# Performance work log

Measured on AMD Instinct MI355X. Metric: run time of the kernel, lower is better.

The kernel has to match this reference:

```python
import jax, jax.numpy as jnp
import numpy as np

D_K = 64

def setup_inputs() -> dict:
    key = jax.random.key(0)
    k1, k2, k3, k4 = jax.random.split(key, 4)
    hidden_states = jax.random.normal(k1, (2, 16, 128, 16, 16), dtype=jnp.float32)
    # nn.Linear(hidden, d, bias=False); stored as [in, out] for x @ W
    w_q = jax.random.normal(k2, (128, 64), dtype=jnp.float32) * 0.05
    w_k = jax.random.normal(k3, (128, 64), dtype=jnp.float32) * 0.05
    w_v = jax.random.normal(k4, (128, 64), dtype=jnp.float32) * 0.05
    return {"hidden_states": hidden_states, "w_q": w_q, "w_k": w_k, "w_v": w_v}

def reference(hidden_states, w_q, w_k, w_v):
    # (B, T, C, H, W) -> (B, T, H, W, C) -> (N, C)
    x = jnp.transpose(hidden_states, (0, 1, 3, 4, 2))
    x = x.reshape(-1, x.shape[-1])                      # [N, C], N = B*T*H*W
    q = x @ w_q                                          # [N, d_k]
    k = x @ w_k                                          # [N, d_k]
    v = x @ w_v                                          # [N, d_v]
    scores = (q @ k.T) / jnp.sqrt(jnp.asarray(D_K, x.dtype))  # [N, N]
    attn = jax.nn.softmax(scores, axis=1)                # softmax over dim=1
    out = attn @ v                                       # [N, d_v]
    return out
```

## Files before the change

kernel.cpp:

```cpp
#include <hip/hip_runtime.h>
#include <hip/hip_bf16.h>

typedef float f32x4 __attribute__((ext_vector_type(4)));
typedef short bf16x8 __attribute__((ext_vector_type(8)));

#define MFMA32 __builtin_amdgcn_mfma_f32_16x16x32_bf16

__device__ __forceinline__ unsigned short f2bf(float f) {
  union { float f; unsigned u; } v; v.f = f;
  unsigned u = v.u;
  u += 0x7FFFu + ((u >> 16) & 1u);
  return (unsigned short)(u >> 16);
}

__device__ __forceinline__ bf16x8 pack8_bf16(float a, float b, float c, float d,
                                             float e, float f, float g, float h) {
  union { bf16x8 v; __hip_bfloat162 p[4]; } u;
  u.p[0] = __float22bfloat162_rn(make_float2(a, b));
  u.p[1] = __float22bfloat162_rn(make_float2(c, d));
  u.p[2] = __float22bfloat162_rn(make_float2(e, f));
  u.p[3] = __float22bfloat162_rn(make_float2(g, h));
  return u.v;
}

__device__ __forceinline__ void stage16(const unsigned short* gbase,
                                        unsigned short* lbase, int lane) {
#if __has_builtin(__builtin_amdgcn_global_load_lds)
  __builtin_amdgcn_global_load_lds(
      (const __attribute__((address_space(1))) void*)(gbase + lane * 8),
      (__attribute__((address_space(3))) void*)lbase, 16, 0, 0);
#else
  *(bf16x8*)(lbase + lane * 8) = *(const bf16x8*)(gbase + lane * 8);
#endif
}

__global__ __launch_bounds__(256) void qkv_kernel(
    const float* __restrict__ hs,
    const float* __restrict__ wq, const float* __restrict__ wk,
    const float* __restrict__ wv,
    unsigned short* __restrict__ qb, unsigned short* __restrict__ kpack,
    unsigned short* __restrict__ vpack)
{
  __shared__ __align__(16) float Wl[128 * 64];
  __shared__ float xs[32 * 129];
  const int t = threadIdx.x;
  const int mat = blockIdx.y;
  const float* __restrict__ W = (mat == 0) ? wq : (mat == 1) ? wk : wv;
  #pragma unroll
  for (int i = 0; i < 8; ++i) {
    *(f32x4*)(Wl + i * 1024 + t * 4) = *(const f32x4*)(W + i * 1024 + t * 4);
  }
  const int n0 = blockIdx.x * 32;
  const int bt = n0 >> 8;
  const int sp0 = n0 & 255;
  {
    const float* __restrict__ src = hs + (size_t)bt * 32768 + sp0;
    const int s = t & 31, cb = t >> 5;
    #pragma unroll
    for (int i = 0; i < 16; ++i) {
      const int c = i * 8 + cb;
      xs[s * 129 + c] = src[c * 256 + s];
    }
  }
  __syncthreads();
  const int s = t & 31, g = t >> 5;
  float acc[8];
  #pragma unroll
  for (int j = 0; j < 8; ++j) acc[j] = 0.f;
  #pragma unroll 4
  for (int c = 0; c < 128; ++c) {
    const float xv = xs[s * 129 + c];
    const f32x4 w0 = *(const f32x4*)(Wl + c * 64 + g * 8);
    const f32x4 w1 = *(const f32x4*)(Wl + c * 64 + g * 8 + 4);
    acc[0] += xv * w0[0]; acc[1] += xv * w0[1];
    acc[2] += xv * w0[2]; acc[3] += xv * w0[3];
    acc[4] += xv * w1[0]; acc[5] += xv * w1[1];
    acc[6] += xv * w1[2]; acc[7] += xv * w1[3];
  }
  const int n = n0 + s;
  const float SCALE = 1.4426950408889634f / 8.0f;
  if (mat == 0) {
    #pragma unroll
    for (int j = 0; j < 8; ++j) qb[n * 64 + g * 8 + j] = f2bf(acc[j] * SCALE);
  } else if (mat == 1) {
    const int kvb32 = n >> 5, kvl = n & 31;
    const int ti = (kvl >> 2) & 1;
    const int lowk = ((kvl >> 3) << 2) | (kvl & 3);
    const int h = g >> 2, quadk = g & 3;
    unsigned short* dst =
        kpack + (((size_t)(kvb32 * 2 + ti) * 2 + h) * 64 + quadk * 16 + lowk) * 8;
    #pragma unroll
    for (int j = 0; j < 8; ++j) dst[j] = f2bf(acc[j]);
  } else {
    const int kvb32 = n >> 5, kvl = n & 31;
    const int quadv = kvl >> 3, jj = kvl & 7;
    #pragma unroll
    for (int jw = 0; jw < 8; ++jw) {
      const int d = g * 8 + jw, dt = d >> 4, lowd = d & 15;
      vpack[(((size_t)kvb32 * 4 + dt) * 64 + quadv * 16 + lowd) * 8 + jj] =
          f2bf(acc[jw]);
    }
  }
}

__global__ __launch_bounds__(256, 2) void flash_kernel(
    const unsigned short* __restrict__ qb,
    const unsigned short* __restrict__ kpack,
    const unsigned short* __restrict__ vpack,
    float* __restrict__ opart, float* __restrict__ lpart, int kvlen)
{
  __shared__ __align__(16) unsigned short Kl[2][4][2048];
  __shared__ __align__(16) unsigned short Vl[2][4][2048];
  const int t = threadIdx.x;
  const int w = t >> 6, lane = t & 63;
  const int quad = lane >> 4, low = lane & 15;
  const int bid = blockIdx.x;
  const int q0 = (bid & 31) * 256 + w * 64;
  const int g = bid >> 5;
  const int kvb32_0 = (g * kvlen) >> 5;
  const int nch = kvlen >> 7;

  bf16x8 bq[4][2];
  #pragma unroll
  for (int qt = 0; qt < 4; ++qt)
    #pragma unroll
    for (int h = 0; h < 2; ++h)
      bq[qt][h] = *(const bf16x8*)(qb + (q0 + qt * 16 + low) * 64 + h * 32 + quad * 8);

  f32x4 O[4][4];
  f32x4 O4[4];
  #pragma unroll
  for (int qt = 0; qt < 4; ++qt) {
    #pragma unroll
    for (int dt = 0; dt < 4; ++dt) O[qt][dt] = (f32x4){0.f, 0.f, 0.f, 0.f};
    O4[qt] = (f32x4){0.f, 0.f, 0.f, 0.f};
  }
  const bf16x8 ones = {16256, 16256, 16256, 16256, 16256, 16256, 16256, 16256};

  #define STAGE_CHUNK(b, c)                                                   \
    {                                                                         \
      const size_t kb = (size_t)(kvb32_0 + (c) * 4 + w) * 2048;               \
      _Pragma("unroll")                                                       \
      for (int r = 0; r < 4; ++r) {                                           \
        stage16(kpack + kb + r * 512, &Kl[b][w][r * 512], lane);              \
        stage16(vpack + kb + r * 512, &Vl[b][w][r * 512], lane);              \
      }                                                                       \
    }

  STAGE_CHUNK(0, 0)
  __syncthreads();

  for (int c = 0; c < nch; ++c) {
    const int b = c & 1;
    if (c + 1 < nch) STAGE_CHUNK(b ^ 1, c + 1)
    #pragma unroll
    for (int j = 0; j < 4; ++j) {
      bf16x8 kf[4], vf[4];
      #pragma unroll
      for (int f = 0; f < 4; ++f)
        kf[f] = *(const bf16x8*)&Kl[b][j][f * 512 + lane * 8];
      #pragma unroll
      for (int f = 0; f < 4; ++f)
        vf[f] = *(const bf16x8*)&Vl[b][j][f * 512 + lane * 8];
      #pragma unroll
      for (int qt = 0; qt < 4; ++qt) {
        f32x4 SA = {0.f, 0.f, 0.f, 0.f}, SB = {0.f, 0.f, 0.f, 0.f};
        SA = MFMA32(kf[0], bq[qt][0], SA, 0, 0, 0);
        SA = MFMA32(kf[1], bq[qt][1], SA, 0, 0, 0);
        SB = MFMA32(kf[2], bq[qt][0], SB, 0, 0, 0);
        SB = MFMA32(kf[3], bq[qt][1], SB, 0, 0, 0);
        const float pa0 = __builtin_amdgcn_exp2f(SA[0]);
        const float pa1 = __builtin_amdgcn_exp2f(SA[1]);
        const float pa2 = __builtin_amdgcn_exp2f(SA[2]);
        const float pa3 = __builtin_amdgcn_exp2f(SA[3]);
        const float pb0 = __builtin_amdgcn_exp2f(SB[0]);
        const float pb1 = __builtin_amdgcn_exp2f(SB[1]);
        const float pb2 = __builtin_amdgcn_exp2f(SB[2]);
        const float pb3 = __builtin_amdgcn_exp2f(SB[3]);
        const bf16x8 pf = pack8_bf16(pa0, pa1, pa2, pa3, pb0, pb1, pb2, pb3);
        #pragma unroll
        for (int dt = 0; dt < 4; ++dt)
          O[qt][dt] = MFMA32(vf[dt], pf, O[qt][dt], 0, 0, 0);
        O4[qt] = MFMA32(ones, pf, O4[qt], 0, 0, 0);
      }
    }
    __syncthreads();
  }

  #pragma unroll
  for (int qt = 0; qt < 4; ++qt) {
    const size_t qrow = (size_t)g * 8192 + q0 + qt * 16;
    #pragma unroll
    for (int dt = 0; dt < 4; ++dt)
      *(f32x4*)(opart + (qrow + low) * 64 + dt * 16 + quad * 4) = O[qt][dt];
    if (quad == 0) lpart[qrow + low] = O4[qt][0];
  }
}

__global__ __launch_bounds__(256) void reduce_kernel(
    const float* __restrict__ opart, const float* __restrict__ lpart,
    float* __restrict__ out, int G)
{
  const int idx = blockIdx.x * 256 + threadIdx.x;
  const int q = idx >> 4;
  const int d4 = (idx & 15) * 4;
  float den = 0.f;
  f32x4 num = {0.f, 0.f, 0.f, 0.f};
  for (int g = 0; g < G; ++g) {
    den += lpart[g * 8192 + q];
    const f32x4 o = *(const f32x4*)(opart + ((size_t)g * 8192 + q) * 64 + d4);
    num[0] += o[0]; num[1] += o[1]; num[2] += o[2]; num[3] += o[3];
  }
  const float r = 1.0f / den;
  f32x4 res = {num[0] * r, num[1] * r, num[2] * r, num[3] * r};
  *(f32x4*)(out + (size_t)q * 64 + d4) = res;
}

extern "C" void kernel_launch(void* const* d_in, const int* in_sizes, int n_in,
                              void* d_out, int out_size, void* d_ws, size_t ws_size,
                              hipStream_t stream) {
  const float* hs = (const float*)d_in[0];
  const float* wq = (const float*)d_in[1];
  const float* wk = (const float*)d_in[2];
  const float* wv = (const float*)d_in[3];
  float* out = (float*)d_out;
  char* ws = (char*)d_ws;

  unsigned short* qb    = (unsigned short*)ws;
  unsigned short* kpack = (unsigned short*)(ws + (1 << 20));
  unsigned short* vpack = (unsigned short*)(ws + (2 << 20));

  int G = 16;
  {
    const size_t per_g = (size_t)8192 * 64 * 4 + (size_t)8192 * 4;
    while (G > 1 && ws_size < (size_t)(3 << 20) + (size_t)G * per_g) G >>= 1;
  }
  float* opart = (float*)(ws + (3 << 20));
  float* lpart = (float*)(ws + (3 << 20) + (size_t)G * 8192 * 64 * 4);

  qkv_kernel<<<dim3(256, 3, 1), 256, 0, stream>>>(hs, wq, wk, wv, qb, kpack, vpack);
  flash_kernel<<<32 * G, 256, 0, stream>>>(qb, kpack, vpack, opart, lpart, 8192 / G);
  reduce_kernel<<<512, 256, 0, stream>>>(opart, lpart, out, G);
}
```

Baseline: 98.49 us.

## Fuse QKV, flash and reduce into one cooperative persistent kernel

```diff
diff --git a/kernel.cpp b/kernel.cpp
--- a/kernel.cpp
+++ b/kernel.cpp
@@ -1,5 +1,8 @@
 #include <hip/hip_runtime.h>
 #include <hip/hip_bf16.h>
+#include <hip/hip_cooperative_groups.h>
+
+namespace cg = cooperative_groups;
 
 typedef float f32x4 __attribute__((ext_vector_type(4)));
 typedef short bf16x8 __attribute__((ext_vector_type(8)));
@@ -34,23 +37,30 @@
 #endif
 }
 
-__global__ __launch_bounds__(256) void qkv_kernel(
+struct QkvSmem {
+  float Wl[128 * 64];
+  float xs[32 * 129];
+};
+struct FlashSmem {
+  unsigned short Kl[2][4][2048];
+  unsigned short Vl[2][4][2048];
+};
+union FusedSmem { QkvSmem q; FlashSmem f; };
+
+__device__ __forceinline__ void qkv_body(
+    QkvSmem& sm, int mat, int xb, int t,
     const float* __restrict__ hs,
     const float* __restrict__ wq, const float* __restrict__ wk,
     const float* __restrict__ wv,
     unsigned short* __restrict__ qb, unsigned short* __restrict__ kpack,
     unsigned short* __restrict__ vpack)
 {
-  __shared__ __align__(16) float Wl[128 * 64];
-  __shared__ float xs[32 * 129];
-  const int t = threadIdx.x;
-  const int mat = blockIdx.y;
   const float* __restrict__ W = (mat == 0) ? wq : (mat == 1) ? wk : wv;
   #pragma unroll
   for (int i = 0; i < 8; ++i) {
-    *(f32x4*)(Wl + i * 1024 + t * 4) = *(const f32x4*)(W + i * 1024 + t * 4);
-  }
-  const int n0 = blockIdx.x * 32;
+    *(f32x4*)(sm.Wl + i * 1024 + t * 4) = *(const f32x4*)(W + i * 1024 + t * 4);
+  }
+  const int n0 = xb * 32;
   const int bt = n0 >> 8;
   const int sp0 = n0 & 255;
   {
@@ -59,7 +69,7 @@
     #pragma unroll
     for (int i = 0; i < 16; ++i) {
       const int c = i * 8 + cb;
-      xs[s * 129 + c] = src[c * 256 + s];
+      sm.xs[s * 129 + c] = src[c * 256 + s];
     }
   }
   __syncthreads();
@@ -69,9 +79,9 @@
   for (int j = 0; j < 8; ++j) acc[j] = 0.f;
   #pragma unroll 4
   for (int c = 0; c < 128; ++c) {
-    const float xv = xs[s * 129 + c];
-    const f32x4 w0 = *(const f32x4*)(Wl + c * 64 + g * 8);
-    const f32x4 w1 = *(const f32x4*)(Wl + c * 64 + g * 8 + 4);
+    const float xv = sm.xs[s * 129 + c];
+    const f32x4 w0 = *(const f32x4*)(sm.Wl + c * 64 + g * 8);
+    const f32x4 w1 = *(const f32x4*)(sm.Wl + c * 64 + g * 8 + 4);
     acc[0] += xv * w0[0]; acc[1] += xv * w0[1];
     acc[2] += xv * w0[2]; acc[3] += xv * w0[3];
     acc[4] += xv * w1[0]; acc[5] += xv * w1[1];
@@ -103,20 +113,17 @@
   }
 }
 
-__global__ __launch_bounds__(256, 2) void flash_kernel(
+__device__ __forceinline__ void flash_body(
+    FlashSmem& sm, int fb, int t,
     const unsigned short* __restrict__ qb,
     const unsigned short* __restrict__ kpack,
     const unsigned short* __restrict__ vpack,
     float* __restrict__ opart, float* __restrict__ lpart, int kvlen)
 {
-  __shared__ __align__(16) unsigned short Kl[2][4][2048];
-  __shared__ __align__(16) unsigned short Vl[2][4][2048];
-  const int t = threadIdx.x;
   const int w = t >> 6, lane = t & 63;
   const int quad = lane >> 4, low = lane & 15;
-  const int bid = blockIdx.x;
-  const int q0 = (bid & 31) * 256 + w * 64;
-  const int g = bid >> 5;
+  const int q0 = (fb & 31) * 256 + w * 64;
+  const int g = fb >> 5;
   const int kvb32_0 = (g * kvlen) >> 5;
   const int nch = kvlen >> 7;
 
@@ -128,22 +135,21 @@
       bq[qt][h] = *(const bf16x8*)(qb + (q0 + qt * 16 + low) * 64 + h * 32 + quad * 8);
 
   f32x4 O[4][4];
-  f32x4 O4[4];
+  float la[4];
   #pragma unroll
   for (int qt = 0; qt < 4; ++qt) {
     #pragma unroll
     for (int dt = 0; dt < 4; ++dt) O[qt][dt] = (f32x4){0.f, 0.f, 0.f, 0.f};
-    O4[qt] = (f32x4){0.f, 0.f, 0.f, 0.f};
-  }
-  const bf16x8 ones = {16256, 16256, 16256, 16256, 16256, 16256, 16256, 16256};
+    la[qt] = 0.f;
+  }
 
   #define STAGE_CHUNK(b, c)                                                   \
     {                                                                         \
       const size_t kb = (size_t)(kvb32_0 + (c) * 4 + w) * 2048;               \
       _Pragma("unroll")                                                       \
       for (int r = 0; r < 4; ++r) {                                           \
-        stage16(kpack + kb + r * 512, &Kl[b][w][r * 512], lane);              \
-        stage16(vpack + kb + r * 512, &Vl[b][w][r * 512], lane);              \
+        stage16(kpack + kb + r * 512, &sm.Kl[b][w][r * 512], lane);           \
+        stage16(vpack + kb + r * 512, &sm.Vl[b][w][r * 512], lane);           \
       }                                                                       \
     }
 
@@ -158,10 +164,10 @@
       bf16x8 kf[4], vf[4];
       #pragma unroll
       for (int f = 0; f < 4; ++f)
-        kf[f] = *(const bf16x8*)&Kl[b][j][f * 512 + lane * 8];
+        kf[f] = *(const bf16x8*)&sm.Kl[b][j][f * 512 + lane * 8];
       #pragma unroll
       for (int f = 0; f < 4; ++f)
-        vf[f] = *(const bf16x8*)&Vl[b][j][f * 512 + lane * 8];
+        vf[f] = *(const bf16x8*)&sm.Vl[b][j][f * 512 + lane * 8];
       #pragma unroll
       for (int qt = 0; qt < 4; ++qt) {
         f32x4 SA = {0.f, 0.f, 0.f, 0.f}, SB = {0.f, 0.f, 0.f, 0.f};
@@ -177,11 +183,11 @@
         const float pb1 = __builtin_amdgcn_exp2f(SB[1]);
         const float pb2 = __builtin_amdgcn_exp2f(SB[2]);
         const float pb3 = __builtin_amdgcn_exp2f(SB[3]);
+        la[qt] += ((pa0 + pa1) + (pa2 + pa3)) + ((pb0 + pb1) + (pb2 + pb3));
         const bf16x8 pf = pack8_bf16(pa0, pa1, pa2, pa3, pb0, pb1, pb2, pb3);
         #pragma unroll
         for (int dt = 0; dt < 4; ++dt)
           O[qt][dt] = MFMA32(vf[dt], pf, O[qt][dt], 0, 0, 0);
-        O4[qt] = MFMA32(ones, pf, O4[qt], 0, 0, 0);
       }
     }
     __syncthreads();
@@ -193,27 +199,100 @@
     #pragma unroll
     for (int dt = 0; dt < 4; ++dt)
       *(f32x4*)(opart + (qrow + low) * 64 + dt * 16 + quad * 4) = O[qt][dt];
-    if (quad == 0) lpart[qrow + low] = O4[qt][0];
-  }
+    float l = la[qt];
+    l += __shfl_xor(l, 16);
+    l += __shfl_xor(l, 32);
+    if (quad == 0) lpart[qrow + low] = l;
+  }
+  #undef STAGE_CHUNK
+}
+
+__device__ __forceinline__ void reduce_body(
+    int idx, int G, const float* __restrict__ opart,
+    const float* __restrict__ lpart, float* __restrict__ out)
+{
+  const int q = idx >> 4;
+  const int d4 = (idx & 15) * 4;
+  f32x4 n0 = {0.f, 0.f, 0.f, 0.f}, n1 = n0, n2 = n0, n3 = n0;
+  float d0 = 0.f, d1 = 0.f, d2 = 0.f, d3 = 0.f;
+  int g = 0;
+  for (; g + 4 <= G; g += 4) {
+    const size_t r0 = (size_t)(g + 0) * 8192 + q;
+    const size_t r1 = (size_t)(g + 1) * 8192 + q;
+    const size_t r2 = (size_t)(g + 2) * 8192 + q;
+    const size_t r3 = (size_t)(g + 3) * 8192 + q;
+    d0 += lpart[r0]; d1 += lpart[r1]; d2 += lpart[r2]; d3 += lpart[r3];
+    n0 += *(const f32x4*)(opart + r0 * 64 + d4);
+    n1 += *(const f32x4*)(opart + r1 * 64 + d4);
+    n2 += *(const f32x4*)(opart + r2 * 64 + d4);
+    n3 += *(const f32x4*)(opart + r3 * 64 + d4);
+  }
+  for (; g < G; ++g) {
+    const size_t r0 = (size_t)g * 8192 + q;
+    d0 += lpart[r0];
+    n0 += *(const f32x4*)(opart + r0 * 64 + d4);
+  }
+  const float den = (d0 + d1) + (d2 + d3);
+  const f32x4 num = (n0 + n1) + (n2 + n3);
+  const float r = 1.0f / den;
+  *(f32x4*)(out + (size_t)q * 64 + d4) = num * r;
+}
+
+__global__ __launch_bounds__(256, 2) void fused_kernel(
+    const float* __restrict__ hs,
+    const float* __restrict__ wq, const float* __restrict__ wk,
+    const float* __restrict__ wv,
+    unsigned short* __restrict__ qb, unsigned short* __restrict__ kpack,
+    unsigned short* __restrict__ vpack,
+    float* __restrict__ opart, float* __restrict__ lpart,
+    float* __restrict__ out, int G)
+{
+  __shared__ __align__(16) FusedSmem sm;
+  const int t = threadIdx.x;
+  const int bid = blockIdx.x;
+  const int nb = gridDim.x;
+
+  for (int u = bid; u < 768; u += nb) {
+    __syncthreads();
+    qkv_body(sm.q, u >> 8, u & 255, t, hs, wq, wk, wv, qb, kpack, vpack);
+  }
+  cg::this_grid().sync();
+
+  const int kvlen = 8192 / G;
+  for (int fb = bid; fb < 32 * G; fb += nb)
+    flash_body(sm.f, fb, t, qb, kpack, vpack, opart, lpart, kvlen);
+  cg::this_grid().sync();
+
+  for (int idx = bid * 256 + t; idx < 131072; idx += nb * 256)
+    reduce_body(idx, G, opart, lpart, out);
+}
+
+__global__ __launch_bounds__(256) void qkv_kernel(
+    const float* __restrict__ hs,
+    const float* __restrict__ wq, const float* __restrict__ wk,
+    const float* __restrict__ wv,
+    unsigned short* __restrict__ qb, unsigned short* __restrict__ kpack,
+    unsigned short* __restrict__ vpack)
+{
+  __shared__ __align__(16) QkvSmem sm;
+  qkv_body(sm, blockIdx.y, blockIdx.x, threadIdx.x, hs, wq, wk, wv, qb, kpack, vpack);
+}
+
+__global__ __launch_bounds__(256, 2) void flash_kernel(
+    const unsigned short* __restrict__ qb,
+    const unsigned short* __restrict__ kpack,
+    const unsigned short* __restrict__ vpack,
+    float* __restrict__ opart, float* __restrict__ lpart, int kvlen)
+{
+  __shared__ __align__(16) FlashSmem sm;
+  flash_body(sm, blockIdx.x, threadIdx.x, qb, kpack, vpack, opart, lpart, kvlen);
 }
 
 __global__ __launch_bounds__(256) void reduce_kernel(
     const float* __restrict__ opart, const float* __restrict__ lpart,
     float* __restrict__ out, int G)
 {
-  const int idx = blockIdx.x * 256 + threadIdx.x;
-  const int q = idx >> 4;
-  const int d4 = (idx & 15) * 4;
-  float den = 0.f;
-  f32x4 num = {0.f, 0.f, 0.f, 0.f};
-  for (int g = 0; g < G; ++g) {
-    den += lpart[g * 8192 + q];
-    const f32x4 o = *(const f32x4*)(opart + ((size_t)g * 8192 + q) * 64 + d4);
-    num[0] += o[0]; num[1] += o[1]; num[2] += o[2]; num[3] += o[3];
-  }
-  const float r = 1.0f / den;
-  f32x4 res = {num[0] * r, num[1] * r, num[2] * r, num[3] * r};
-  *(f32x4*)(out + (size_t)q * 64 + d4) = res;
+  reduce_body(blockIdx.x * 256 + (int)threadIdx.x, G, opart, lpart, out);
 }
 
 extern "C" void kernel_launch(void* const* d_in, const int* in_sizes, int n_in,
@@ -238,7 +317,17 @@
   float* opart = (float*)(ws + (3 << 20));
   float* lpart = (float*)(ws + (3 << 20) + (size_t)G * 8192 * 64 * 4);
 
-  qkv_kernel<<<dim3(256, 3, 1), 256, 0, stream>>>(hs, wq, wk, wv, qb, kpack, vpack);
-  flash_kernel<<<32 * G, 256, 0, stream>>>(qb, kpack, vpack, opart, lpart, 8192 / G);
-  reduce_kernel<<<512, 256, 0, stream>>>(opart, lpart, out, G);
-}
+  int nb = 32 * G;
+  if (nb > 512) nb = 512;
+
+  void* args[] = {(void*)&hs, (void*)&wq, (void*)&wk, (void*)&wv,
+                  (void*)&qb, (void*)&kpack, (void*)&vpack,
+                  (void*)&opart, (void*)&lpart, (void*)&out, (void*)&G};
+  hipError_t e = hipLaunchCooperativeKernel(
+      reinterpret_cast<void*>(fused_kernel), dim3(nb), dim3(256), args, 0, stream);
+  if (e != hipSuccess) {
+    qkv_kernel<<<dim3(256, 3, 1), 256, 0, stream>>>(hs, wq, wk, wv, qb, kpack, vpack);
+    flash_kernel<<<32 * G, 256, 0, stream>>>(qb, kpack, vpack, opart, lpart, 8192 / G);
+    reduce_kernel<<<512, 256, 0, stream>>>(opart, lpart, out, G);
+  }
+}
```

Measured after the change: 286.2 us. +190.5%, slower.
